# Kernel optimization log

Measured on AMD Instinct MI355X. Metric: run time of the kernel, lower is better.

## Reference

```python
import jax, jax.numpy as jnp
import numpy as np

H = 8  # pinyin_feature_size = embedding_dim = GRU hidden size
VOCAB = 27


def setup_inputs() -> dict:
    key = jax.random.key(0)
    ks = jax.random.split(key, 10)
    B, T = 131072, 24
    inputs = jax.random.randint(ks[0], (B, T), 0, VOCAB, dtype=jnp.int32)
    emb = jax.random.normal(ks[1], (VOCAB, H), dtype=jnp.float32)
    emb = emb.at[0].set(0.0)  # padding_idx=0
    s = 0.25  # ~ 1/sqrt(hidden) init scale like torch GRU
    w_ih1 = jax.random.normal(ks[2], (3 * H, H), dtype=jnp.float32) * s
    w_hh1 = jax.random.normal(ks[3], (3 * H, H), dtype=jnp.float32) * s
    b_ih1 = jax.random.normal(ks[4], (3 * H,), dtype=jnp.float32) * s
    b_hh1 = jax.random.normal(ks[5], (3 * H,), dtype=jnp.float32) * s
    w_ih2 = jax.random.normal(ks[6], (3 * H, H), dtype=jnp.float32) * s
    w_hh2 = jax.random.normal(ks[7], (3 * H, H), dtype=jnp.float32) * s
    b_ih2 = jax.random.normal(ks[8], (3 * H,), dtype=jnp.float32) * s
    b_hh2 = jax.random.normal(ks[9], (3 * H,), dtype=jnp.float32) * s
    return {"inputs": inputs, "emb": emb,
            "w_ih1": w_ih1, "w_hh1": w_hh1, "b_ih1": b_ih1, "b_hh1": b_hh1,
            "w_ih2": w_ih2, "w_hh2": w_hh2, "b_ih2": b_ih2, "b_hh2": b_hh2}


def _gru_layer(x_seq, w_ih, w_hh, b_ih, b_hh):
    # x_seq: [B, T, H_in] -> all hidden states [B, T, H], final h [B, H]
    B = x_seq.shape[0]
    # precompute input-side gates for all timesteps: [T, B, 3H]
    gi_all = jnp.einsum('bti,gi->tbg', x_seq, w_ih) + b_ih
    h0 = jnp.zeros((B, H), dtype=x_seq.dtype)

    def cell(h, gi):
        gh = h @ w_hh.T + b_hh  # [B, 3H]
        i_r, i_z, i_n = jnp.split(gi, 3, axis=-1)
        h_r, h_z, h_n = jnp.split(gh, 3, axis=-1)
        r = jax.nn.sigmoid(i_r + h_r)
        z = jax.nn.sigmoid(i_z + h_z)
        n = jnp.tanh(i_n + r * h_n)
        h_new = (1.0 - z) * n + z * h
        return h_new, h_new

    h_last, hs = jax.lax.scan(cell, h0, gi_all)
    return jnp.swapaxes(hs, 0, 1), h_last  # [B, T, H], [B, H]


def reference(inputs, emb, w_ih1, w_hh1, b_ih1, b_hh1,
              w_ih2, w_hh2, b_ih2, b_hh2):
    # padding_idx=0 => row 0 of the table is zero
    emb_eff = emb.at[0].set(0.0)
    x = emb_eff[inputs]  # [B, T, H]
    h1_seq, _ = _gru_layer(x, w_ih1, w_hh1, b_ih1, b_hh1)
    # dropout(0.15) between layers is inactive in eval mode
    _, h2_last = _gru_layer(h1_seq, w_ih2, w_hh2, b_ih2, b_hh2)
    return h2_last  # [B, H] == output[1][-1]
```

## Files before the change

### kernel.cpp

```cpp
#include <hip/hip_runtime.h>


typedef __fp16 h2f   __attribute__((ext_vector_type(2)));
typedef __fp16 half8 __attribute__((ext_vector_type(8)));
typedef float  f32x16 __attribute__((ext_vector_type(16)));

#define LOG2E 1.44269504088896f

__device__ __forceinline__ h2f pk2(float a, float b) {
  return __builtin_amdgcn_cvt_pkrtz(a, b);
}

union H8U { half8 h; unsigned u[4]; h2f p[4]; };

__global__ __launch_bounds__(256, 4) void gru2_mfma(
    const int* __restrict__ inputs,
    const float* __restrict__ emb,
    const float* __restrict__ w_ih1, const float* __restrict__ w_hh1,
    const float* __restrict__ b_ih1, const float* __restrict__ b_hh1,
    const float* __restrict__ w_ih2, const float* __restrict__ w_hh2,
    const float* __restrict__ b_ih2, const float* __restrict__ b_hh2,
    float* __restrict__ out)
{
  __shared__ float G1f[27 * 26];
  __shared__ int   TK[128 * 25];

  const int tid   = threadIdx.x;
  const int lane  = tid & 63;
  const int wid   = tid >> 6;
  const int half_ = lane >> 5;
  const int col   = lane & 31;

  for (int idx = tid; idx < 27 * 24; idx += 256) {
    const int tok = idx / 24, g = idx - tok * 24;
    const float s = (g < 16) ? -LOG2E : 2.f * LOG2E;
    float a = b_ih1[g] + ((g < 16) ? b_hh1[g] : 0.f);
    if (tok != 0) {
      #pragma unroll
      for (int j = 0; j < 8; ++j) a = fmaf(w_ih1[g * 8 + j], emb[tok * 8 + j], a);
    }
    G1f[tok * 26 + g] = s * a;
  }

  const long gbase = (long)blockIdx.x * (128 * 24);
  #pragma unroll
  for (int k = 0; k < 12; ++k) {
    const int i = tid + k * 256;
    TK[(i / 24) * 25 + (i % 24)] = inputs[gbase + i];
  }
  __syncthreads();

  const int sl = wid * 32 + col;
  unsigned pkw[4] = {0u, 0u, 0u, 0u};
  #pragma unroll
  for (int t = 0; t < 24; ++t)
    pkw[t / 6] |= ((unsigned)TK[sl * 25 + t]) << (5 * (t % 6));
  const unsigned pk0 = pkw[0], pk1 = pkw[1], pk2_ = pkw[2], pk3 = pkw[3];

  auto loadW = [&](const float* w) -> half8 {
    H8U u;
    u.u[0] = u.u[1] = u.u[2] = u.u[3] = 0u;
    if (half_ == 0 && col < 24) {
      const float s = (col < 16) ? -LOG2E : 2.f * LOG2E;
      const float4* p = (const float4*)(w + col * 8);
      const float4 x = p[0], y = p[1];
      u.p[0] = pk2(x.x * s, x.y * s);
      u.p[1] = pk2(x.z * s, x.w * s);
      u.p[2] = pk2(y.x * s, y.y * s);
      u.p[3] = pk2(y.z * s, y.w * s);
    }
    return u.h;
  };
  const half8 wa1  = loadW(w_hh1);
  const half8 wa2i = loadW(w_ih2);
  const half8 wa2h = loadW(w_hh2);

  f32x16 c2;
  #pragma unroll
  for (int r = 0; r < 16; ++r) {
    const int m = (r & 3) + 8 * (r >> 2) + 4 * half_;
    float v;
    if (m < 16)      v = -LOG2E * (b_ih2[m] + b_hh2[m]);
    else if (m < 24) v = 2.f * LOG2E * b_hh2[m];
    else             v = 0.f;
    c2[r] = v;
  }
  float bn1[4], bi2n[4];
  #pragma unroll
  for (int i = 0; i < 4; ++i) {
    bn1[i]  = 2.f * LOG2E * b_hh1[16 + 4 * half_ + i];
    bi2n[i] = 2.f * LOG2E * b_ih2[16 + 4 * half_ + i];
  }

  float h1v[4] = {0.f, 0.f, 0.f, 0.f}, h2v[4] = {0.f, 0.f, 0.f, 0.f};
  H8U f1, f2;
  f1.u[0] = f1.u[1] = f1.u[2] = f1.u[3] = 0u;
  f2 = f1;

  const float* g1base = G1f + half_ * 4;
  const int pidx = (lane ^ 32) << 2;

  for (int g = 0; g < 4; ++g) {
    unsigned pw = pk0;
    if (g == 1) pw = pk1;
    if (g == 2) pw = pk2_;
    if (g == 3) pw = pk3;

    #pragma unroll
    for (int j = 0; j < 6; ++j) {
      const unsigned tok = (pw >> (5 * j)) & 31u;
      const float* gp = g1base + tok * 26;
      const float2 a01 = *(const float2*)(gp + 0);
      const float2 a23 = *(const float2*)(gp + 2);
      const float2 z01 = *(const float2*)(gp + 8);
      const float2 z23 = *(const float2*)(gp + 10);
      const float2 n01 = *(const float2*)(gp + 16);
      const float2 n23 = *(const float2*)(gp + 18);

      f32x16 c1;
      c1[0] = a01.x; c1[1] = a01.y; c1[2] = a23.x; c1[3] = a23.y;
      c1[4] = z01.x; c1[5] = z01.y; c1[6] = z23.x; c1[7] = z23.y;
      c1[8] = bn1[0]; c1[9] = bn1[1]; c1[10] = bn1[2]; c1[11] = bn1[3];
      c1[12] = 0.f; c1[13] = 0.f; c1[14] = 0.f; c1[15] = 0.f;

      const f32x16 d1 = __builtin_amdgcn_mfma_f32_32x32x16_f16(wa1, f1.h, c1, 0, 0, 0);

      const float gin1[4] = {n01.x, n01.y, n23.x, n23.y};
      #pragma unroll
      for (int i = 0; i < 4; ++i) {
        const float r = __builtin_amdgcn_rcpf(1.f + __builtin_amdgcn_exp2f(d1[i]));
        const float z = __builtin_amdgcn_rcpf(1.f + __builtin_amdgcn_exp2f(d1[4 + i]));
        const float na = fmaf(r, d1[8 + i], gin1[i]);
        const float n = fmaf(-2.f, __builtin_amdgcn_rcpf(1.f + __builtin_amdgcn_exp2f(na)), 1.f);
        h1v[i] = n + z * (h1v[i] - n);
      }
      {
        const unsigned a = __builtin_bit_cast(unsigned, pk2(h1v[0], h1v[1]));
        const unsigned b = __builtin_bit_cast(unsigned, pk2(h1v[2], h1v[3]));
        f1.u[0] = a; f1.u[1] = b;
        f1.u[2] = (unsigned)__builtin_amdgcn_ds_bpermute(pidx, (int)a);
        f1.u[3] = (unsigned)__builtin_amdgcn_ds_bpermute(pidx, (int)b);
      }

      const f32x16 dh = __builtin_amdgcn_mfma_f32_32x32x16_f16(wa2h, f2.h, c2, 0, 0, 0);
      const f32x16 dg = __builtin_amdgcn_mfma_f32_32x32x16_f16(wa2i, f1.h, dh, 0, 0, 0);

      #pragma unroll
      for (int i = 0; i < 4; ++i) {
        const float r = __builtin_amdgcn_rcpf(1.f + __builtin_amdgcn_exp2f(dg[i]));
        const float z = __builtin_amdgcn_rcpf(1.f + __builtin_amdgcn_exp2f(dg[4 + i]));
        const float gin = dg[8 + i] - dh[8 + i] + bi2n[i];
        const float na = fmaf(r, dh[8 + i], gin);
        const float n = fmaf(-2.f, __builtin_amdgcn_rcpf(1.f + __builtin_amdgcn_exp2f(na)), 1.f);
        h2v[i] = n + z * (h2v[i] - n);
      }
      {
        const unsigned a = __builtin_bit_cast(unsigned, pk2(h2v[0], h2v[1]));
        const unsigned b = __builtin_bit_cast(unsigned, pk2(h2v[2], h2v[3]));
        f2.u[0] = a; f2.u[1] = b;
        f2.u[2] = (unsigned)__builtin_amdgcn_ds_bpermute(pidx, (int)a);
        f2.u[3] = (unsigned)__builtin_amdgcn_ds_bpermute(pidx, (int)b);
      }
    }
  }

  const long seq = (long)blockIdx.x * 128 + sl;
  *(float4*)(out + seq * 8 + 4 * half_) =
      make_float4(h2v[0], h2v[1], h2v[2], h2v[3]);
}

extern "C" void kernel_launch(void* const* d_in, const int* in_sizes, int n_in,
                              void* d_out, int out_size, void* d_ws, size_t ws_size,
                              hipStream_t stream) {
  const int*   inputs = (const int*)d_in[0];
  const float* emb    = (const float*)d_in[1];
  const float* w_ih1  = (const float*)d_in[2];
  const float* w_hh1  = (const float*)d_in[3];
  const float* b_ih1  = (const float*)d_in[4];
  const float* b_hh1  = (const float*)d_in[5];
  const float* w_ih2  = (const float*)d_in[6];
  const float* w_hh2  = (const float*)d_in[7];
  const float* b_ih2  = (const float*)d_in[8];
  const float* b_hh2  = (const float*)d_in[9];
  float* out = (float*)d_out;

  const int B = in_sizes[0] / 24;
  const int grid = B / 128;

  hipLaunchKernelGGL(gru2_mfma, dim3(grid), dim3(256), 0, stream,
                     inputs, emb, w_ih1, w_hh1, b_ih1, b_hh1,
                     w_ih2, w_hh2, b_ih2, b_hh2, out);
}
```

Baseline: 111.7 us.

## Software-pipeline GRU layers across timesteps and use permlane32 swap for half exchange

Restructures the timestep loop so the layer-1 MFMA for step t+1 is issued right after layer-1 h is produced. It then overlaps with the layer-2 gate math for step t, and the layer-2 hidden MFMA is issued early. The next token's gate table entries are prefetched one step ahead. The LDS-based ds_bpermute half-swap is replaced with permlane32_swap. The gate table stride is padded to 33 to reduce bank conflicts on the token-indexed gather. Full unrolling of 24 steps raises register pressure and code size.

```diff
diff --git a/kernel.cpp b/kernel.cpp
--- a/kernel.cpp
+++ b/kernel.cpp
@@ -1,17 +1,22 @@
 #include <hip/hip_runtime.h>
 
 
-typedef __fp16 h2f   __attribute__((ext_vector_type(2)));
-typedef __fp16 half8 __attribute__((ext_vector_type(8)));
+typedef __fp16 h2f    __attribute__((ext_vector_type(2)));
+typedef __fp16 half8  __attribute__((ext_vector_type(8)));
 typedef float  f32x16 __attribute__((ext_vector_type(16)));
 
 #define LOG2E 1.44269504088896f
 
-__device__ __forceinline__ h2f pk2(float a, float b) {
+__device__ __forceinline__ h2f pk2f(float a, float b) {
   return __builtin_amdgcn_cvt_pkrtz(a, b);
 }
 
 union H8U { half8 h; unsigned u[4]; h2f p[4]; };
+
+__device__ __forceinline__ unsigned from_upper(unsigned x) {
+  auto r = __builtin_amdgcn_permlane32_swap((int)x, (int)x, false, false);
+  return (unsigned)r[1];
+}
 
 __global__ __launch_bounds__(256, 4) void gru2_mfma(
     const int* __restrict__ inputs,
@@ -22,7 +27,7 @@
     const float* __restrict__ b_ih2, const float* __restrict__ b_hh2,
     float* __restrict__ out)
 {
-  __shared__ float G1f[27 * 26];
+  __shared__ float G1f[27 * 33];
   __shared__ int   TK[128 * 25];
 
   const int tid   = threadIdx.x;
@@ -39,7 +44,7 @@
       #pragma unroll
       for (int j = 0; j < 8; ++j) a = fmaf(w_ih1[g * 8 + j], emb[tok * 8 + j], a);
     }
-    G1f[tok * 26 + g] = s * a;
+    G1f[tok * 33 + g] = s * a;
   }
 
   const long gbase = (long)blockIdx.x * (128 * 24);
@@ -56,6 +61,11 @@
   for (int t = 0; t < 24; ++t)
     pkw[t / 6] |= ((unsigned)TK[sl * 25 + t]) << (5 * (t % 6));
   const unsigned pk0 = pkw[0], pk1 = pkw[1], pk2_ = pkw[2], pk3 = pkw[3];
+
+  auto tok_at = [&](int t) -> unsigned {
+    const unsigned pw = (t < 6) ? pk0 : (t < 12) ? pk1 : (t < 18) ? pk2_ : pk3;
+    return (pw >> (5 * (t % 6))) & 31u;
+  };
 
   auto loadW = [&](const float* w) -> half8 {
     H8U u;
@@ -64,10 +74,10 @@
       const float s = (col < 16) ? -LOG2E : 2.f * LOG2E;
       const float4* p = (const float4*)(w + col * 8);
       const float4 x = p[0], y = p[1];
-      u.p[0] = pk2(x.x * s, x.y * s);
-      u.p[1] = pk2(x.z * s, x.w * s);
-      u.p[2] = pk2(y.x * s, y.y * s);
-      u.p[3] = pk2(y.z * s, y.w * s);
+      u.p[0] = pk2f(x.x * s, x.y * s);
+      u.p[1] = pk2f(x.z * s, x.w * s);
+      u.p[2] = pk2f(y.x * s, y.y * s);
+      u.p[3] = pk2f(y.z * s, y.w * s);
     }
     return u.h;
   };
@@ -98,69 +108,69 @@
   f2 = f1;
 
   const float* g1base = G1f + half_ * 4;
-  const int pidx = (lane ^ 32) << 2;
-
-  for (int g = 0; g < 4; ++g) {
-    unsigned pw = pk0;
-    if (g == 1) pw = pk1;
-    if (g == 2) pw = pk2_;
-    if (g == 3) pw = pk3;
+
+  f32x16 c1;
+  c1[8] = bn1[0]; c1[9] = bn1[1]; c1[10] = bn1[2]; c1[11] = bn1[3];
+  c1[12] = 0.f; c1[13] = 0.f; c1[14] = 0.f; c1[15] = 0.f;
+  float gin1[4];
+  {
+    const float* gp = g1base + tok_at(0) * 33;
+    c1[0] = gp[0];  c1[1] = gp[1];  c1[2] = gp[2];  c1[3] = gp[3];
+    c1[4] = gp[8];  c1[5] = gp[9];  c1[6] = gp[10]; c1[7] = gp[11];
+    gin1[0] = gp[16]; gin1[1] = gp[17]; gin1[2] = gp[18]; gin1[3] = gp[19];
+  }
+  f32x16 d1 = c1;
+
+  #pragma unroll
+  for (int t = 0; t < 24; ++t) {
+    float nc[8], ng[4];
+    if (t < 23) {
+      const float* gp = g1base + tok_at(t + 1) * 33;
+      nc[0] = gp[0];  nc[1] = gp[1];  nc[2] = gp[2];  nc[3] = gp[3];
+      nc[4] = gp[8];  nc[5] = gp[9];  nc[6] = gp[10]; nc[7] = gp[11];
+      ng[0] = gp[16]; ng[1] = gp[17]; ng[2] = gp[18]; ng[3] = gp[19];
+    }
+
+    const f32x16 dh = __builtin_amdgcn_mfma_f32_32x32x16_f16(wa2h, f2.h, c2, 0, 0, 0);
 
     #pragma unroll
-    for (int j = 0; j < 6; ++j) {
-      const unsigned tok = (pw >> (5 * j)) & 31u;
-      const float* gp = g1base + tok * 26;
-      const float2 a01 = *(const float2*)(gp + 0);
-      const float2 a23 = *(const float2*)(gp + 2);
-      const float2 z01 = *(const float2*)(gp + 8);
-      const float2 z23 = *(const float2*)(gp + 10);
-      const float2 n01 = *(const float2*)(gp + 16);
-      const float2 n23 = *(const float2*)(gp + 18);
-
-      f32x16 c1;
-      c1[0] = a01.x; c1[1] = a01.y; c1[2] = a23.x; c1[3] = a23.y;
-      c1[4] = z01.x; c1[5] = z01.y; c1[6] = z23.x; c1[7] = z23.y;
-      c1[8] = bn1[0]; c1[9] = bn1[1]; c1[10] = bn1[2]; c1[11] = bn1[3];
-      c1[12] = 0.f; c1[13] = 0.f; c1[14] = 0.f; c1[15] = 0.f;
-
-      const f32x16 d1 = __builtin_amdgcn_mfma_f32_32x32x16_f16(wa1, f1.h, c1, 0, 0, 0);
-
-      const float gin1[4] = {n01.x, n01.y, n23.x, n23.y};
-      #pragma unroll
-      for (int i = 0; i < 4; ++i) {
-        const float r = __builtin_amdgcn_rcpf(1.f + __builtin_amdgcn_exp2f(d1[i]));
-        const float z = __builtin_amdgcn_rcpf(1.f + __builtin_amdgcn_exp2f(d1[4 + i]));
-        const float na = fmaf(r, d1[8 + i], gin1[i]);
-        const float n = fmaf(-2.f, __builtin_amdgcn_rcpf(1.f + __builtin_amdgcn_exp2f(na)), 1.f);
-        h1v[i] = n + z * (h1v[i] - n);
-      }
-      {
-        const unsigned a = __builtin_bit_cast(unsigned, pk2(h1v[0], h1v[1]));
-        const unsigned b = __builtin_bit_cast(unsigned, pk2(h1v[2], h1v[3]));
-        f1.u[0] = a; f1.u[1] = b;
-        f1.u[2] = (unsigned)__builtin_amdgcn_ds_bpermute(pidx, (int)a);
-        f1.u[3] = (unsigned)__builtin_amdgcn_ds_bpermute(pidx, (int)b);
-      }
-
-      const f32x16 dh = __builtin_amdgcn_mfma_f32_32x32x16_f16(wa2h, f2.h, c2, 0, 0, 0);
-      const f32x16 dg = __builtin_amdgcn_mfma_f32_32x32x16_f16(wa2i, f1.h, dh, 0, 0, 0);
-
-      #pragma unroll
-      for (int i = 0; i < 4; ++i) {
-        const float r = __builtin_amdgcn_rcpf(1.f + __builtin_amdgcn_exp2f(dg[i]));
-        const float z = __builtin_amdgcn_rcpf(1.f + __builtin_amdgcn_exp2f(dg[4 + i]));
-        const float gin = dg[8 + i] - dh[8 + i] + bi2n[i];
-        const float na = fmaf(r, dh[8 + i], gin);
-        const float n = fmaf(-2.f, __builtin_amdgcn_rcpf(1.f + __builtin_amdgcn_exp2f(na)), 1.f);
-        h2v[i] = n + z * (h2v[i] - n);
-      }
-      {
-        const unsigned a = __builtin_bit_cast(unsigned, pk2(h2v[0], h2v[1]));
-        const unsigned b = __builtin_bit_cast(unsigned, pk2(h2v[2], h2v[3]));
-        f2.u[0] = a; f2.u[1] = b;
-        f2.u[2] = (unsigned)__builtin_amdgcn_ds_bpermute(pidx, (int)a);
-        f2.u[3] = (unsigned)__builtin_amdgcn_ds_bpermute(pidx, (int)b);
-      }
+    for (int i = 0; i < 4; ++i) {
+      const float r = __builtin_amdgcn_rcpf(1.f + __builtin_amdgcn_exp2f(d1[i]));
+      const float z = __builtin_amdgcn_rcpf(1.f + __builtin_amdgcn_exp2f(d1[4 + i]));
+      const float na = fmaf(r, d1[8 + i], gin1[i]);
+      const float n = fmaf(-2.f, __builtin_amdgcn_rcpf(1.f + __builtin_amdgcn_exp2f(na)), 1.f);
+      h1v[i] = n + z * (h1v[i] - n);
+    }
+    {
+      const unsigned a = __builtin_bit_cast(unsigned, pk2f(h1v[0], h1v[1]));
+      const unsigned b = __builtin_bit_cast(unsigned, pk2f(h1v[2], h1v[3]));
+      f1.u[0] = a; f1.u[1] = b;
+      f1.u[2] = from_upper(a); f1.u[3] = from_upper(b);
+    }
+
+    const f32x16 dg = __builtin_amdgcn_mfma_f32_32x32x16_f16(wa2i, f1.h, dh, 0, 0, 0);
+
+    if (t < 23) {
+      c1[0] = nc[0]; c1[1] = nc[1]; c1[2] = nc[2]; c1[3] = nc[3];
+      c1[4] = nc[4]; c1[5] = nc[5]; c1[6] = nc[6]; c1[7] = nc[7];
+      gin1[0] = ng[0]; gin1[1] = ng[1]; gin1[2] = ng[2]; gin1[3] = ng[3];
+      d1 = __builtin_amdgcn_mfma_f32_32x32x16_f16(wa1, f1.h, c1, 0, 0, 0);
+    }
+
+    #pragma unroll
+    for (int i = 0; i < 4; ++i) {
+      const float r = __builtin_amdgcn_rcpf(1.f + __builtin_amdgcn_exp2f(dg[i]));
+      const float z = __builtin_amdgcn_rcpf(1.f + __builtin_amdgcn_exp2f(dg[4 + i]));
+      const float gin = dg[8 + i] - dh[8 + i] + bi2n[i];
+      const float na = fmaf(r, dh[8 + i], gin);
+      const float n = fmaf(-2.f, __builtin_amdgcn_rcpf(1.f + __builtin_amdgcn_exp2f(na)), 1.f);
+      h2v[i] = n + z * (h2v[i] - n);
+    }
+    {
+      const unsigned a = __builtin_bit_cast(unsigned, pk2f(h2v[0], h2v[1]));
+      const unsigned b = __builtin_bit_cast(unsigned, pk2f(h2v[2], h2v[3]));
+      f2.u[0] = a; f2.u[1] = b;
+      f2.u[2] = from_upper(a); f2.u[3] = from_upper(b);
     }
   }
 
```

Result: no change. 112.2 us (+0.4%).
